# Kernel tuning notes

Hardware: AMD Instinct MI355X
Metric: run time of the kernel (lower is better)

Reference implementation:

```python
import jax, jax.numpy as jnp
import numpy as np

B, L, H, NUM_LABELS = 4, 256, 768, 13


def setup_inputs() -> dict:
    key = jax.random.key(0)
    k1, k2, k3, k4, k5 = jax.random.split(key, 5)
    s1 = 1.0 / np.sqrt(2 * H)
    s2 = 1.0 / np.sqrt(H)
    return {
        "hidden_states": jax.random.normal(k1, (B, L, H), dtype=jnp.float32),
        "W1": jax.random.uniform(k2, (2 * H, H), jnp.float32, -s1, s1),
        "b1": jax.random.uniform(k3, (H,), jnp.float32, -s1, s1),
        "W2": jax.random.uniform(k4, (H, NUM_LABELS), jnp.float32, -s2, s2),
        "b2": jax.random.uniform(k5, (NUM_LABELS,), jnp.float32, -s2, s2),
    }


def reference(hidden_states, W1, b1, W2, b2):
    # Original: ffn(cat([x_start expand over dim2, x_end expand over dim1], -1))
    # Algebraically: Linear(2H->H) on the concat == proj(x_start) + proj(x_end)
    # broadcast over the L x L span grid, avoiding the (B,L,L,2H) tensor.
    H_ = hidden_states.shape[-1]
    xs_proj = jnp.einsum('bsh,hk->bsk', hidden_states, W1[:H_])   # start half
    xe_proj = jnp.einsum('bsh,hk->bsk', hidden_states, W1[H_:])   # end half
    h = xs_proj[:, :, None, :] + xe_proj[:, None, :, :] + b1      # (B,L,L,H)
    h = jax.nn.gelu(h, approximate=False)                         # torch GELU default = exact erf
    logits = jnp.einsum('bijk,kn->bijn', h, W2) + b2              # (B,L,L,num_labels)
    return logits
```

## Files before the change

### kernel.cpp

```cpp
#include <hip/hip_runtime.h>
#include <math.h>

#define H 768
#define L 256
#define NB 4
#define NL 13

typedef _Float16 h2 __attribute__((ext_vector_type(2)));
typedef _Float16 half8 __attribute__((ext_vector_type(8)));
typedef float f32x4 __attribute__((ext_vector_type(4)));

__device__ inline h2 gelu_pk(h2 x) {
    const _Float16 kC = (_Float16)3.75f;
    h2 hi = {kC, kC}, lo = {(_Float16)-3.75f, (_Float16)-3.75f};
    h2 xc = __builtin_elementwise_min(__builtin_elementwise_max(x, lo), hi);
    h2 u = xc * xc;
    const _Float16 kE = (_Float16)0.125f;
    h2 ve = {kE, kE};
    h2 v = u * ve;
    const _Float16 d4v = (_Float16)0.0832840f,  d3v = (_Float16)-0.4335206f;
    const _Float16 d2v = (_Float16)0.8960128f,  d1v = (_Float16)-0.9876456f;
    const _Float16 d0v = (_Float16)0.7946463f;
    h2 d4 = {d4v, d4v}, d3 = {d3v, d3v}, d2 = {d2v, d2v}, d1 = {d1v, d1v}, d0 = {d0v, d0v};
    h2 p = v * (v * (v * (v * d4 + d3) + d2) + d1) + d0;
    h2 t = xc * p;
    const _Float16 kH = (_Float16)0.5f;
    h2 halfv = {kH, kH};
    h2 hx = x * halfv;
    return hx * t + hx;
}

__global__ __launch_bounds__(256) void prep_kernel(
    const float* __restrict__ X, const float* __restrict__ W1,
    const float* __restrict__ W2,
    _Float16* __restrict__ Afrag, _Float16* __restrict__ Bfrag1,
    _Float16* __restrict__ Bfrag2)
{
    __shared__ __align__(16) unsigned char smem[16 * 784 * 2];
    const int blk = blockIdx.x;
    const int tid = threadIdx.x;

    if (blk < 64) {
        _Float16* T = (_Float16*)smem;
        const int mt = blk;
        const int row = tid >> 4, colg = tid & 15;
        #pragma unroll
        for (int cc = 0; cc < 12; ++cc) {
            int c4 = (colg + cc * 16) * 4;
            float4 f = *(const float4*)&X[(size_t)(mt * 16 + row) * H + c4];
            _Float16* d = T + row * 784 + c4;
            d[0] = (_Float16)f.x; d[1] = (_Float16)f.y;
            d[2] = (_Float16)f.z; d[3] = (_Float16)f.w;
        }
        __syncthreads();
        #pragma unroll
        for (int rr = 0; rr < 12; ++rr) {
            int kb = rr * 2 + (tid >> 7);
            int sub = tid & 127;
            int lane = sub >> 1, u4 = (sub & 1) * 4;
            int ln = lane & 15, q = lane >> 4;
            const _Float16* s = T + ln * 784 + kb * 32 + q * 8 + u4;
            ushort4 o = { *(const unsigned short*)&s[0], *(const unsigned short*)&s[1],
                          *(const unsigned short*)&s[2], *(const unsigned short*)&s[3] };
            *(ushort4*)&Afrag[(((size_t)mt * 24 + kb) * 64 + lane) * 8 + u4] = o;
        }
    } else if (blk < 64 + 1152) {
        _Float16* T = (_Float16*)smem;
        const int t2 = blk - 64;
        const int kb = t2 % 24, ng = t2 / 24;
        const int n0p = ng * 32;
        const float* Wb = W1 + ((n0p >= H) ? (size_t)H * H : 0);
        const int c0 = n0p - ((n0p >= H) ? H : 0);
        const int row = tid >> 3, c4 = (tid & 7) * 4;
        float4 f = *(const float4*)&Wb[(size_t)(kb * 32 + row) * H + c0 + c4];
        _Float16* d = T + row * 36 + c4;
        d[0] = (_Float16)f.x; d[1] = (_Float16)f.y;
        d[2] = (_Float16)f.z; d[3] = (_Float16)f.w;
        __syncthreads();
        int u4 = (tid & 1) * 4;
        int lane = (tid >> 1) & 63;
        int nts = tid >> 7;
        int ln = lane & 15, q = lane >> 4;
        ushort4 o;
        unsigned short* os = (unsigned short*)&o;
        #pragma unroll
        for (int i = 0; i < 4; ++i)
            os[i] = *(const unsigned short*)&T[(q * 8 + u4 + i) * 36 + nts * 16 + ln];
        int ntg = (n0p >> 4) + nts;
        *(ushort4*)&Bfrag1[(((size_t)ntg * 24 + kb) * 64 + lane) * 8 + u4] = o;
    } else {
        int base = (blk - 64 - 1152) * 768 + tid;
        #pragma unroll
        for (int r = 0; r < 3; ++r) {
            int idx = base + r * 256;
            int u = idx & 7;
            int lane = (idx >> 3) & 63;
            int kb = idx >> 9;
            int k = kb * 32 + ((lane >> 4) << 3) + u;
            int n = lane & 15;
            float v = (n < NL) ? W2[(size_t)k * NL + n] : 0.f;
            Bfrag2[idx] = (_Float16)v;
        }
    }
}

__global__ __launch_bounds__(256) void gemm_mfma(
    const _Float16* __restrict__ Afrag, const _Float16* __restrict__ Bfrag1,
    const float* __restrict__ b1, _Float16* __restrict__ Pxs2,
    _Float16* __restrict__ Pxe)
{
    const int tid = threadIdx.x;
    const int w = tid >> 6, lane = tid & 63;
    const int ln = lane & 15, quad = lane >> 4;
    const int m0 = blockIdx.x * 64 + (w & 1) * 32;
    const int n0g = blockIdx.y * 64 + (w >> 1) * 32;
    const int mt0 = m0 >> 4, ntg0 = n0g >> 4;

    const half8* pa0 = (const half8*)(Afrag + (((size_t)mt0 * 24) * 64 + lane) * 8);
    const half8* pa1 = (const half8*)(Afrag + ((((size_t)mt0 + 1) * 24) * 64 + lane) * 8);
    const half8* pb0 = (const half8*)(Bfrag1 + (((size_t)ntg0 * 24) * 64 + lane) * 8);
    const half8* pb1 = (const half8*)(Bfrag1 + ((((size_t)ntg0 + 1) * 24) * 64 + lane) * 8);

    f32x4 acc[2][2] = {};
    #pragma unroll 4
    for (int kb = 0; kb < 24; ++kb) {
        half8 a0 = pa0[kb * 64];
        half8 a1 = pa1[kb * 64];
        half8 b0 = pb0[kb * 64];
        half8 b1v = pb1[kb * 64];
        acc[0][0] = __builtin_amdgcn_mfma_f32_16x16x32_f16(a0, b0, acc[0][0], 0, 0, 0);
        acc[0][1] = __builtin_amdgcn_mfma_f32_16x16x32_f16(a0, b1v, acc[0][1], 0, 0, 0);
        acc[1][0] = __builtin_amdgcn_mfma_f32_16x16x32_f16(a1, b0, acc[1][0], 0, 0, 0);
        acc[1][1] = __builtin_amdgcn_mfma_f32_16x16x32_f16(a1, b1v, acc[1][1], 0, 0, 0);
    }

    if (n0g < H) {
        float bv[2] = { b1[n0g + ln], b1[n0g + 16 + ln] };
        #pragma unroll
        for (int mt = 0; mt < 2; ++mt)
            #pragma unroll
            for (int nt = 0; nt < 2; ++nt) {
                int n = n0g + nt * 16 + ln;
                #pragma unroll
                for (int r = 0; r < 4; ++r) {
                    int m = m0 + mt * 16 + quad * 4 + r;
                    Pxs2[(size_t)m * H + n] = (_Float16)(acc[mt][nt][r] + bv[nt]);
                }
            }
    } else {
        #pragma unroll
        for (int mt = 0; mt < 2; ++mt)
            #pragma unroll
            for (int nt = 0; nt < 2; ++nt) {
                int n = n0g - H + nt * 16 + ln;
                #pragma unroll
                for (int r = 0; r < 4; ++r) {
                    int m = m0 + mt * 16 + quad * 4 + r;
                    Pxe[(size_t)m * H + n] = (_Float16)acc[mt][nt][r];
                }
            }
    }
}

__global__ __launch_bounds__(256, 6) void span_mfma_kernel(
    const _Float16* __restrict__ Pxs2, const _Float16* __restrict__ Pxe,
    const _Float16* __restrict__ Bfrag2, const float* __restrict__ b2,
    float* __restrict__ out)
{
    __shared__ unsigned int xs2[H / 2];
    const int bi = blockIdx.x >> 1;
    const int jh = blockIdx.x & 1;
    const int b = bi >> 8;
    const int tid = threadIdx.x;
    const unsigned int* xrow = (const unsigned int*)(Pxs2 + (size_t)bi * H);
    for (int t = tid; t < H / 2; t += 256) xs2[t] = xrow[t];

    const int wave = tid >> 6;
    const int lane = tid & 63;
    const int n = lane & 15;
    const int quad = lane >> 4;
    const int j_base = jh * 128 + wave * 32;

    const _Float16* xerow[2];
    #pragma unroll
    for (int t = 0; t < 2; ++t)
        xerow[t] = Pxe + (size_t)(b * L + j_base + t * 16 + n) * H;

    f32x4 acc[2] = {};
    __syncthreads();

    for (int kb = 0; kb < H / 32; ++kb) {
        const int k8 = kb * 32 + quad * 8;
        half8 bfrag = *(const half8*)(Bfrag2 + ((size_t)kb * 64 + lane) * 8);
        uint4 xsd = *(const uint4*)&xs2[k8 >> 1];
        h2 xsp[4] = { __builtin_bit_cast(h2, xsd.x), __builtin_bit_cast(h2, xsd.y),
                      __builtin_bit_cast(h2, xsd.z), __builtin_bit_cast(h2, xsd.w) };

        #pragma unroll
        for (int t = 0; t < 2; ++t) {
            uint4 xev = *(const uint4*)(xerow[t] + k8);
            h2 xep[4] = { __builtin_bit_cast(h2, xev.x), __builtin_bit_cast(h2, xev.y),
                          __builtin_bit_cast(h2, xev.z), __builtin_bit_cast(h2, xev.w) };
            unsigned int pk[4];
            #pragma unroll
            for (int p = 0; p < 4; ++p) {
                h2 g = gelu_pk(xsp[p] + xep[p]);
                pk[p] = __builtin_bit_cast(unsigned int, g);
            }
            uint4 pk4 = {pk[0], pk[1], pk[2], pk[3]};
            half8 afrag = __builtin_bit_cast(half8, pk4);
            acc[t] = __builtin_amdgcn_mfma_f32_16x16x32_f16(afrag, bfrag, acc[t], 0, 0, 0);
        }
    }

    if (n < NL) {
        float b2v = b2[n];
        #pragma unroll
        for (int t = 0; t < 2; ++t)
            #pragma unroll
            for (int r = 0; r < 4; ++r) {
                int j = j_base + t * 16 + quad * 4 + r;
                out[((size_t)bi * L + j) * NL + n] = acc[t][r] + b2v;
            }
    }
}

extern "C" void kernel_launch(void* const* d_in, const int* in_sizes, int n_in,
                              void* d_out, int out_size, void* d_ws, size_t ws_size,
                              hipStream_t stream)
{
    (void)in_sizes; (void)n_in; (void)out_size; (void)ws_size;
    const float* X  = (const float*)d_in[0];
    const float* W1 = (const float*)d_in[1];
    const float* b1 = (const float*)d_in[2];
    const float* W2 = (const float*)d_in[3];
    const float* b2 = (const float*)d_in[4];
    float* out = (float*)d_out;

    char* ws = (char*)d_ws;
    _Float16* Pxs2   = (_Float16*)ws;
    _Float16* Pxe    = Pxs2 + (size_t)NB * L * H;
    _Float16* Afrag  = Pxe + (size_t)NB * L * H;
    _Float16* Bfrag1 = Afrag + (size_t)NB * L * H;
    _Float16* Bfrag2 = Bfrag1 + (size_t)2 * H * H;

    prep_kernel<<<64 + 1152 + 16, 256, 0, stream>>>(X, W1, W2, Afrag, Bfrag1, Bfrag2);
    gemm_mfma<<<dim3(16, 24), 256, 0, stream>>>(Afrag, Bfrag1, b1, Pxs2, Pxe);
    span_mfma_kernel<<<NB * L * 2, 256, 0, stream>>>(Pxs2, Pxe, Bfrag2, b2, out);
}
```

Before: 134.8 us.

## Fuse fp16 conversion into projection GEMM and widen span kernel per block

Removes the separate prep kernel by having the projection GEMM convert X on the fly and transpose a W1 column slab into shared memory, with one extra block row packing W2 fragments. The span kernel now processes a full 256-column row per block (4 tiles per wave), with register double-buffering of the next Pxe chunk, and its occupancy hint drops from 6 to 4. This saves a launch and the fragment round trip through global memory, and reuses the shared xs row across more outputs. The cost is more register pressure, fewer blocks, and redundant fp32 X reads across the 48 column blocks.

```diff
diff --git a/kernel.cpp b/kernel.cpp
--- a/kernel.cpp
+++ b/kernel.cpp
@@ -30,69 +30,18 @@
     return hx * t + hx;
 }
 
-__global__ __launch_bounds__(256) void prep_kernel(
+__global__ __launch_bounds__(256) void fused_gemm(
     const float* __restrict__ X, const float* __restrict__ W1,
-    const float* __restrict__ W2,
-    _Float16* __restrict__ Afrag, _Float16* __restrict__ Bfrag1,
+    const float* __restrict__ b1, const float* __restrict__ W2,
+    _Float16* __restrict__ Pxs2, _Float16* __restrict__ Pxe,
     _Float16* __restrict__ Bfrag2)
 {
-    __shared__ __align__(16) unsigned char smem[16 * 784 * 2];
-    const int blk = blockIdx.x;
     const int tid = threadIdx.x;
 
-    if (blk < 64) {
-        _Float16* T = (_Float16*)smem;
-        const int mt = blk;
-        const int row = tid >> 4, colg = tid & 15;
-        #pragma unroll
-        for (int cc = 0; cc < 12; ++cc) {
-            int c4 = (colg + cc * 16) * 4;
-            float4 f = *(const float4*)&X[(size_t)(mt * 16 + row) * H + c4];
-            _Float16* d = T + row * 784 + c4;
-            d[0] = (_Float16)f.x; d[1] = (_Float16)f.y;
-            d[2] = (_Float16)f.z; d[3] = (_Float16)f.w;
-        }
-        __syncthreads();
-        #pragma unroll
-        for (int rr = 0; rr < 12; ++rr) {
-            int kb = rr * 2 + (tid >> 7);
-            int sub = tid & 127;
-            int lane = sub >> 1, u4 = (sub & 1) * 4;
-            int ln = lane & 15, q = lane >> 4;
-            const _Float16* s = T + ln * 784 + kb * 32 + q * 8 + u4;
-            ushort4 o = { *(const unsigned short*)&s[0], *(const unsigned short*)&s[1],
-                          *(const unsigned short*)&s[2], *(const unsigned short*)&s[3] };
-            *(ushort4*)&Afrag[(((size_t)mt * 24 + kb) * 64 + lane) * 8 + u4] = o;
-        }
-    } else if (blk < 64 + 1152) {
-        _Float16* T = (_Float16*)smem;
-        const int t2 = blk - 64;
-        const int kb = t2 % 24, ng = t2 / 24;
-        const int n0p = ng * 32;
-        const float* Wb = W1 + ((n0p >= H) ? (size_t)H * H : 0);
-        const int c0 = n0p - ((n0p >= H) ? H : 0);
-        const int row = tid >> 3, c4 = (tid & 7) * 4;
-        float4 f = *(const float4*)&Wb[(size_t)(kb * 32 + row) * H + c0 + c4];
-        _Float16* d = T + row * 36 + c4;
-        d[0] = (_Float16)f.x; d[1] = (_Float16)f.y;
-        d[2] = (_Float16)f.z; d[3] = (_Float16)f.w;
-        __syncthreads();
-        int u4 = (tid & 1) * 4;
-        int lane = (tid >> 1) & 63;
-        int nts = tid >> 7;
-        int ln = lane & 15, q = lane >> 4;
-        ushort4 o;
-        unsigned short* os = (unsigned short*)&o;
-        #pragma unroll
-        for (int i = 0; i < 4; ++i)
-            os[i] = *(const unsigned short*)&T[(q * 8 + u4 + i) * 36 + nts * 16 + ln];
-        int ntg = (n0p >> 4) + nts;
-        *(ushort4*)&Bfrag1[(((size_t)ntg * 24 + kb) * 64 + lane) * 8 + u4] = o;
-    } else {
-        int base = (blk - 64 - 1152) * 768 + tid;
-        #pragma unroll
-        for (int r = 0; r < 3; ++r) {
-            int idx = base + r * 256;
+    if (blockIdx.y == 8) {
+        if (blockIdx.x != 0) return;
+        for (int r = 0; r < 48; ++r) {
+            int idx = r * 256 + tid;
             int u = idx & 7;
             int lane = (idx >> 3) & 63;
             int kb = idx >> 9;
@@ -101,40 +50,63 @@
             float v = (n < NL) ? W2[(size_t)k * NL + n] : 0.f;
             Bfrag2[idx] = (_Float16)v;
         }
-    }
-}
-
-__global__ __launch_bounds__(256) void gemm_mfma(
-    const _Float16* __restrict__ Afrag, const _Float16* __restrict__ Bfrag1,
-    const float* __restrict__ b1, _Float16* __restrict__ Pxs2,
-    _Float16* __restrict__ Pxe)
-{
-    const int tid = threadIdx.x;
-    const int w = tid >> 6, lane = tid & 63;
+        return;
+    }
+
+    __shared__ _Float16 Ts[32][776];
+    const int wv = tid >> 6, lane = tid & 63;
     const int ln = lane & 15, quad = lane >> 4;
-    const int m0 = blockIdx.x * 64 + (w & 1) * 32;
-    const int n0g = blockIdx.y * 64 + (w >> 1) * 32;
-    const int mt0 = m0 >> 4, ntg0 = n0g >> 4;
-
-    const half8* pa0 = (const half8*)(Afrag + (((size_t)mt0 * 24) * 64 + lane) * 8);
-    const half8* pa1 = (const half8*)(Afrag + ((((size_t)mt0 + 1) * 24) * 64 + lane) * 8);
-    const half8* pb0 = (const half8*)(Bfrag1 + (((size_t)ntg0 * 24) * 64 + lane) * 8);
-    const half8* pb1 = (const half8*)(Bfrag1 + ((((size_t)ntg0 + 1) * 24) * 64 + lane) * 8);
+    const int n0g = blockIdx.x * 32;
+    const bool isE = (n0g >= H);
+    const float* Wb = W1 + (isE ? (size_t)H * H : 0);
+    const int c0 = isE ? (n0g - H) : n0g;
+    const int m0 = blockIdx.y * 128 + wv * 32;
+
+    #pragma unroll
+    for (int r = 0; r < 24; ++r) {
+        int idx = r * 256 + tid;
+        int k = idx >> 3;
+        int c4 = (idx & 7) << 2;
+        float4 f = *(const float4*)&Wb[(size_t)k * H + c0 + c4];
+        Ts[c4 + 0][k] = (_Float16)f.x;
+        Ts[c4 + 1][k] = (_Float16)f.y;
+        Ts[c4 + 2][k] = (_Float16)f.z;
+        Ts[c4 + 3][k] = (_Float16)f.w;
+    }
+    __syncthreads();
+
+    const float* px0 = X + (size_t)(m0 + ln) * H + quad * 8;
+    const float* px1 = px0 + (size_t)16 * H;
 
     f32x4 acc[2][2] = {};
-    #pragma unroll 4
-    for (int kb = 0; kb < 24; ++kb) {
-        half8 a0 = pa0[kb * 64];
-        half8 a1 = pa1[kb * 64];
-        half8 b0 = pb0[kb * 64];
-        half8 b1v = pb1[kb * 64];
-        acc[0][0] = __builtin_amdgcn_mfma_f32_16x16x32_f16(a0, b0, acc[0][0], 0, 0, 0);
-        acc[0][1] = __builtin_amdgcn_mfma_f32_16x16x32_f16(a0, b1v, acc[0][1], 0, 0, 0);
-        acc[1][0] = __builtin_amdgcn_mfma_f32_16x16x32_f16(a1, b0, acc[1][0], 0, 0, 0);
-        acc[1][1] = __builtin_amdgcn_mfma_f32_16x16x32_f16(a1, b1v, acc[1][1], 0, 0, 0);
-    }
-
-    if (n0g < H) {
+    #pragma unroll 2
+    for (int kb = 0; kb < H / 32; ++kb) {
+        const int k8 = kb * 32 + quad * 8;
+        half8 afr[2];
+        {
+            float4 xa = *(const float4*)(px0 + kb * 32);
+            float4 xb = *(const float4*)(px0 + kb * 32 + 4);
+            half8 a = { (_Float16)xa.x, (_Float16)xa.y, (_Float16)xa.z, (_Float16)xa.w,
+                        (_Float16)xb.x, (_Float16)xb.y, (_Float16)xb.z, (_Float16)xb.w };
+            afr[0] = a;
+            float4 ya = *(const float4*)(px1 + kb * 32);
+            float4 yb = *(const float4*)(px1 + kb * 32 + 4);
+            half8 c = { (_Float16)ya.x, (_Float16)ya.y, (_Float16)ya.z, (_Float16)ya.w,
+                        (_Float16)yb.x, (_Float16)yb.y, (_Float16)yb.z, (_Float16)yb.w };
+            afr[1] = c;
+        }
+        half8 bfr[2];
+        bfr[0] = *(const half8*)&Ts[ln][k8];
+        bfr[1] = *(const half8*)&Ts[16 + ln][k8];
+        #pragma unroll
+        for (int mt = 0; mt < 2; ++mt)
+            #pragma unroll
+            for (int nt = 0; nt < 2; ++nt)
+                acc[mt][nt] = __builtin_amdgcn_mfma_f32_16x16x32_f16(
+                    afr[mt], bfr[nt], acc[mt][nt], 0, 0, 0);
+    }
+
+    if (!isE) {
         float bv[2] = { b1[n0g + ln], b1[n0g + 16 + ln] };
         #pragma unroll
         for (int mt = 0; mt < 2; ++mt)
@@ -162,14 +134,13 @@
     }
 }
 
-__global__ __launch_bounds__(256, 6) void span_mfma_kernel(
+__global__ __launch_bounds__(256, 4) void span_mfma_kernel(
     const _Float16* __restrict__ Pxs2, const _Float16* __restrict__ Pxe,
     const _Float16* __restrict__ Bfrag2, const float* __restrict__ b2,
     float* __restrict__ out)
 {
     __shared__ unsigned int xs2[H / 2];
-    const int bi = blockIdx.x >> 1;
-    const int jh = blockIdx.x & 1;
+    const int bi = blockIdx.x;
     const int b = bi >> 8;
     const int tid = threadIdx.x;
     const unsigned int* xrow = (const unsigned int*)(Pxs2 + (size_t)bi * H);
@@ -179,16 +150,21 @@
     const int lane = tid & 63;
     const int n = lane & 15;
     const int quad = lane >> 4;
-    const int j_base = jh * 128 + wave * 32;
-
-    const _Float16* xerow[2];
+    const int j_base = wave * 64;
+
+    const _Float16* xerow[4];
     #pragma unroll
-    for (int t = 0; t < 2; ++t)
-        xerow[t] = Pxe + (size_t)(b * L + j_base + t * 16 + n) * H;
-
-    f32x4 acc[2] = {};
+    for (int t = 0; t < 4; ++t)
+        xerow[t] = Pxe + (size_t)(b * L + j_base + t * 16 + n) * H + quad * 8;
+
+    f32x4 acc[4] = {};
     __syncthreads();
 
+    uint4 cur[4];
+    #pragma unroll
+    for (int t = 0; t < 4; ++t) cur[t] = *(const uint4*)(xerow[t]);
+
+    #pragma unroll 2
     for (int kb = 0; kb < H / 32; ++kb) {
         const int k8 = kb * 32 + quad * 8;
         half8 bfrag = *(const half8*)(Bfrag2 + ((size_t)kb * 64 + lane) * 8);
@@ -196,11 +172,16 @@
         h2 xsp[4] = { __builtin_bit_cast(h2, xsd.x), __builtin_bit_cast(h2, xsd.y),
                       __builtin_bit_cast(h2, xsd.z), __builtin_bit_cast(h2, xsd.w) };
 
-        #pragma unroll
-        for (int t = 0; t < 2; ++t) {
-            uint4 xev = *(const uint4*)(xerow[t] + k8);
-            h2 xep[4] = { __builtin_bit_cast(h2, xev.x), __builtin_bit_cast(h2, xev.y),
-                          __builtin_bit_cast(h2, xev.z), __builtin_bit_cast(h2, xev.w) };
+        const int koff = (kb < H / 32 - 1) ? (kb + 1) * 32 : kb * 32;
+        uint4 nxt[4];
+        #pragma unroll
+        for (int t = 0; t < 4; ++t)
+            nxt[t] = *(const uint4*)(xerow[t] - kb * 32 + koff - 32 + kb * 32 + 32);
+
+        #pragma unroll
+        for (int t = 0; t < 4; ++t) {
+            h2 xep[4] = { __builtin_bit_cast(h2, cur[t].x), __builtin_bit_cast(h2, cur[t].y),
+                          __builtin_bit_cast(h2, cur[t].z), __builtin_bit_cast(h2, cur[t].w) };
             unsigned int pk[4];
             #pragma unroll
             for (int p = 0; p < 4; ++p) {
@@ -210,13 +191,14 @@
             uint4 pk4 = {pk[0], pk[1], pk[2], pk[3]};
             half8 afrag = __builtin_bit_cast(half8, pk4);
             acc[t] = __builtin_amdgcn_mfma_f32_16x16x32_f16(afrag, bfrag, acc[t], 0, 0, 0);
+            cur[t] = nxt[t];
         }
     }
 
     if (n < NL) {
         float b2v = b2[n];
         #pragma unroll
-        for (int t = 0; t < 2; ++t)
+        for (int t = 0; t < 4; ++t)
             #pragma unroll
             for (int r = 0; r < 4; ++r) {
                 int j = j_base + t * 16 + quad * 4 + r;
@@ -240,11 +222,8 @@
     char* ws = (char*)d_ws;
     _Float16* Pxs2   = (_Float16*)ws;
     _Float16* Pxe    = Pxs2 + (size_t)NB * L * H;
-    _Float16* Afrag  = Pxe + (size_t)NB * L * H;
-    _Float16* Bfrag1 = Afrag + (size_t)NB * L * H;
-    _Float16* Bfrag2 = Bfrag1 + (size_t)2 * H * H;
-
-    prep_kernel<<<64 + 1152 + 16, 256, 0, stream>>>(X, W1, W2, Afrag, Bfrag1, Bfrag2);
-    gemm_mfma<<<dim3(16, 24), 256, 0, stream>>>(Afrag, Bfrag1, b1, Pxs2, Pxe);
-    span_mfma_kernel<<<NB * L * 2, 256, 0, stream>>>(Pxs2, Pxe, Bfrag2, b2, out);
-}
+    _Float16* Bfrag2 = Pxe + (size_t)NB * L * H;
+
+    fused_gemm<<<dim3(48, 9), 256, 0, stream>>>(X, W1, b1, W2, Pxs2, Pxe, Bfrag2);
+    span_mfma_kernel<<<NB * L, 256, 0, stream>>>(Pxs2, Pxe, Bfrag2, b2, out);
+}
```

Measured after the change: 145.5 us. 7.9% more time.

## Retile span kernel over two start rows and simplify prep fragment packing

Applied to the files above, without the earlier changes.

The span kernel now gives each block two start rows (i) and 64 end rows (j) instead of one start row and 128 end rows. Each wave loads one xe row fragment per k-step and reuses it across both start rows, with both xs rows staged in shared memory. This cuts global xe traffic per MFMA and lowers the occupancy hint from 6 to 4. The prep kernel drops its shared-memory transposes and has each thread gather and convert one 8-element fragment directly from global memory, which makes the W1 gather strided.

```diff
diff --git a/kernel.cpp b/kernel.cpp
--- a/kernel.cpp
+++ b/kernel.cpp
@@ -36,60 +36,38 @@
     _Float16* __restrict__ Afrag, _Float16* __restrict__ Bfrag1,
     _Float16* __restrict__ Bfrag2)
 {
-    __shared__ __align__(16) unsigned char smem[16 * 784 * 2];
     const int blk = blockIdx.x;
     const int tid = threadIdx.x;
 
-    if (blk < 64) {
-        _Float16* T = (_Float16*)smem;
-        const int mt = blk;
-        const int row = tid >> 4, colg = tid & 15;
-        #pragma unroll
-        for (int cc = 0; cc < 12; ++cc) {
-            int c4 = (colg + cc * 16) * 4;
-            float4 f = *(const float4*)&X[(size_t)(mt * 16 + row) * H + c4];
-            _Float16* d = T + row * 784 + c4;
-            d[0] = (_Float16)f.x; d[1] = (_Float16)f.y;
-            d[2] = (_Float16)f.z; d[3] = (_Float16)f.w;
-        }
-        __syncthreads();
-        #pragma unroll
-        for (int rr = 0; rr < 12; ++rr) {
-            int kb = rr * 2 + (tid >> 7);
-            int sub = tid & 127;
-            int lane = sub >> 1, u4 = (sub & 1) * 4;
-            int ln = lane & 15, q = lane >> 4;
-            const _Float16* s = T + ln * 784 + kb * 32 + q * 8 + u4;
-            ushort4 o = { *(const unsigned short*)&s[0], *(const unsigned short*)&s[1],
-                          *(const unsigned short*)&s[2], *(const unsigned short*)&s[3] };
-            *(ushort4*)&Afrag[(((size_t)mt * 24 + kb) * 64 + lane) * 8 + u4] = o;
-        }
-    } else if (blk < 64 + 1152) {
-        _Float16* T = (_Float16*)smem;
-        const int t2 = blk - 64;
-        const int kb = t2 % 24, ng = t2 / 24;
-        const int n0p = ng * 32;
-        const float* Wb = W1 + ((n0p >= H) ? (size_t)H * H : 0);
-        const int c0 = n0p - ((n0p >= H) ? H : 0);
-        const int row = tid >> 3, c4 = (tid & 7) * 4;
-        float4 f = *(const float4*)&Wb[(size_t)(kb * 32 + row) * H + c0 + c4];
-        _Float16* d = T + row * 36 + c4;
-        d[0] = (_Float16)f.x; d[1] = (_Float16)f.y;
-        d[2] = (_Float16)f.z; d[3] = (_Float16)f.w;
-        __syncthreads();
-        int u4 = (tid & 1) * 4;
-        int lane = (tid >> 1) & 63;
-        int nts = tid >> 7;
-        int ln = lane & 15, q = lane >> 4;
-        ushort4 o;
-        unsigned short* os = (unsigned short*)&o;
-        #pragma unroll
-        for (int i = 0; i < 4; ++i)
-            os[i] = *(const unsigned short*)&T[(q * 8 + u4 + i) * 36 + nts * 16 + ln];
-        int ntg = (n0p >> 4) + nts;
-        *(ushort4*)&Bfrag1[(((size_t)ntg * 24 + kb) * 64 + lane) * 8 + u4] = o;
+    if (blk < 384) {
+        int t = blk * 256 + tid;
+        int lane = t & 63;
+        int g = t >> 6;
+        int kb = g % 24, mt = g / 24;
+        int m = mt * 16 + (lane & 15);
+        int k0 = kb * 32 + (lane >> 4) * 8;
+        const float* px = X + (size_t)m * H + k0;
+        float4 a = *(const float4*)px;
+        float4 b = *(const float4*)(px + 4);
+        half8 o = { (_Float16)a.x, (_Float16)a.y, (_Float16)a.z, (_Float16)a.w,
+                    (_Float16)b.x, (_Float16)b.y, (_Float16)b.z, (_Float16)b.w };
+        *(half8*)(Afrag + (size_t)t * 8) = o;
+    } else if (blk < 960) {
+        int t = (blk - 384) * 256 + tid;
+        int lane = t & 63;
+        int g = t >> 6;
+        int kb = g % 24, ntg = g / 24;
+        int np = ntg * 16 + (lane & 15);
+        int k0 = kb * 32 + (lane >> 4) * 8;
+        const float* Wb = W1 + ((np >= H) ? (size_t)H * H : 0);
+        int c = np - ((np >= H) ? H : 0);
+        half8 o;
+        #pragma unroll
+        for (int u = 0; u < 8; ++u)
+            o[u] = (_Float16)Wb[(size_t)(k0 + u) * H + c];
+        *(half8*)(Bfrag1 + (size_t)t * 8) = o;
     } else {
-        int base = (blk - 64 - 1152) * 768 + tid;
+        int base = (blk - 960) * 768 + tid;
         #pragma unroll
         for (int r = 0; r < 3; ++r) {
             int idx = base + r * 256;
@@ -162,45 +140,45 @@
     }
 }
 
-__global__ __launch_bounds__(256, 6) void span_mfma_kernel(
+__global__ __launch_bounds__(256, 4) void span_mfma_kernel(
     const _Float16* __restrict__ Pxs2, const _Float16* __restrict__ Pxe,
     const _Float16* __restrict__ Bfrag2, const float* __restrict__ b2,
     float* __restrict__ out)
 {
-    __shared__ unsigned int xs2[H / 2];
-    const int bi = blockIdx.x >> 1;
-    const int jh = blockIdx.x & 1;
-    const int b = bi >> 8;
+    __shared__ unsigned int xsf[2 * H / 2];
+    const int ip = blockIdx.x >> 2;
+    const int jq = blockIdx.x & 3;
+    const int bi0 = ip * 2;
+    const int b = bi0 >> 8;
     const int tid = threadIdx.x;
-    const unsigned int* xrow = (const unsigned int*)(Pxs2 + (size_t)bi * H);
-    for (int t = tid; t < H / 2; t += 256) xs2[t] = xrow[t];
+
+    const unsigned int* xsrc = (const unsigned int*)(Pxs2 + (size_t)bi0 * H);
+    for (int t = tid; t < H; t += 256) xsf[t] = xsrc[t];
 
     const int wave = tid >> 6;
     const int lane = tid & 63;
     const int n = lane & 15;
     const int quad = lane >> 4;
-    const int j_base = jh * 128 + wave * 32;
-
-    const _Float16* xerow[2];
-    #pragma unroll
-    for (int t = 0; t < 2; ++t)
-        xerow[t] = Pxe + (size_t)(b * L + j_base + t * 16 + n) * H;
+    const int j_load = jq * 64 + wave * 16 + n;
+
+    const _Float16* xerow = Pxe + (size_t)(b * L + j_load) * H + quad * 8;
+    const half8* bptr = (const half8*)(Bfrag2 + (size_t)lane * 8);
 
     f32x4 acc[2] = {};
     __syncthreads();
 
     for (int kb = 0; kb < H / 32; ++kb) {
-        const int k8 = kb * 32 + quad * 8;
-        half8 bfrag = *(const half8*)(Bfrag2 + ((size_t)kb * 64 + lane) * 8);
-        uint4 xsd = *(const uint4*)&xs2[k8 >> 1];
-        h2 xsp[4] = { __builtin_bit_cast(h2, xsd.x), __builtin_bit_cast(h2, xsd.y),
-                      __builtin_bit_cast(h2, xsd.z), __builtin_bit_cast(h2, xsd.w) };
-
-        #pragma unroll
-        for (int t = 0; t < 2; ++t) {
-            uint4 xev = *(const uint4*)(xerow[t] + k8);
-            h2 xep[4] = { __builtin_bit_cast(h2, xev.x), __builtin_bit_cast(h2, xev.y),
-                          __builtin_bit_cast(h2, xev.z), __builtin_bit_cast(h2, xev.w) };
+        half8 bfrag = bptr[kb * 64];
+        uint4 xev = *(const uint4*)(xerow + kb * 32);
+        h2 xep[4] = { __builtin_bit_cast(h2, xev.x), __builtin_bit_cast(h2, xev.y),
+                      __builtin_bit_cast(h2, xev.z), __builtin_bit_cast(h2, xev.w) };
+        const int xo = kb * 16 + quad * 4;
+
+        #pragma unroll
+        for (int i01 = 0; i01 < 2; ++i01) {
+            uint4 xsd = *(const uint4*)&xsf[i01 * (H / 2) + xo];
+            h2 xsp[4] = { __builtin_bit_cast(h2, xsd.x), __builtin_bit_cast(h2, xsd.y),
+                          __builtin_bit_cast(h2, xsd.z), __builtin_bit_cast(h2, xsd.w) };
             unsigned int pk[4];
             #pragma unroll
             for (int p = 0; p < 4; ++p) {
@@ -209,18 +187,18 @@
             }
             uint4 pk4 = {pk[0], pk[1], pk[2], pk[3]};
             half8 afrag = __builtin_bit_cast(half8, pk4);
-            acc[t] = __builtin_amdgcn_mfma_f32_16x16x32_f16(afrag, bfrag, acc[t], 0, 0, 0);
+            acc[i01] = __builtin_amdgcn_mfma_f32_16x16x32_f16(afrag, bfrag, acc[i01], 0, 0, 0);
         }
     }
 
     if (n < NL) {
         float b2v = b2[n];
         #pragma unroll
-        for (int t = 0; t < 2; ++t)
+        for (int i01 = 0; i01 < 2; ++i01)
             #pragma unroll
             for (int r = 0; r < 4; ++r) {
-                int j = j_base + t * 16 + quad * 4 + r;
-                out[((size_t)bi * L + j) * NL + n] = acc[t][r] + b2v;
+                int j = jq * 64 + wave * 16 + quad * 4 + r;
+                out[((size_t)(bi0 + i01) * L + j) * NL + n] = acc[i01][r] + b2v;
             }
     }
 }
@@ -244,7 +222,7 @@
     _Float16* Bfrag1 = Afrag + (size_t)NB * L * H;
     _Float16* Bfrag2 = Bfrag1 + (size_t)2 * H * H;
 
-    prep_kernel<<<64 + 1152 + 16, 256, 0, stream>>>(X, W1, W2, Afrag, Bfrag1, Bfrag2);
+    prep_kernel<<<976, 256, 0, stream>>>(X, W1, W2, Afrag, Bfrag1, Bfrag2);
     gemm_mfma<<<dim3(16, 24), 256, 0, stream>>>(Afrag, Bfrag1, b1, Pxs2, Pxe);
     span_mfma_kernel<<<NB * L * 2, 256, 0, stream>>>(Pxs2, Pxe, Bfrag2, b2, out);
 }
```

New measurement: 124.6 us. 7.6% less time.
